# Performance work log

Hardware: AMD Instinct MI355X
Metric: run time of the kernel (lower is better)

Reference implementation:

```python
import jax, jax.numpy as jnp
import numpy as np
from jax import lax

POST_NMS_TOP_N = 1000   # cfg[cfg_key].RPN_POST_NMS_TOP_N
NMS_THRESH = 0.7        # cfg[cfg_key].RPN_NMS_THRESH
NEG = -1e9
B, N = 4, 65536


def setup_inputs() -> dict:
    key = jax.random.key(0)
    k0, k1, k2, k3, k4, k5, k6 = jax.random.split(key, 7)
    scores = jax.random.uniform(k0, (B, N), dtype=jnp.float32)
    # small deltas so exp(dw) stays in a realistic range
    bbox_deltas = 0.1 * jax.random.normal(k1, (B, N, 4), dtype=jnp.float32)
    # plausible anchor boxes inside a 1024x1024 image
    cx = jax.random.uniform(k2, (N,), minval=0.0, maxval=1024.0)
    cy = jax.random.uniform(k3, (N,), minval=0.0, maxval=1024.0)
    w = jax.random.uniform(k4, (N,), minval=16.0, maxval=256.0)
    h = jax.random.uniform(k5, (N,), minval=16.0, maxval=256.0)
    anchors = jnp.stack([cx - 0.5 * w, cy - 0.5 * h, cx + 0.5 * w, cy + 0.5 * h], axis=-1).astype(jnp.float32)
    im_info = jnp.tile(jnp.array([[1024.0, 1024.0, 1.0]], dtype=jnp.float32), (B, 1))
    ids = jax.random.randint(k6, (N,), 0, 5, dtype=jnp.int32)  # FPN level ids
    return {"scores": scores, "bbox_deltas": bbox_deltas, "anchors": anchors,
            "im_info": im_info, "ids": ids}


def _iou_one(box, boxes):
    # box [4], boxes [N,4]; mmcv convention (no +1)
    x1 = jnp.maximum(box[0], boxes[:, 0])
    y1 = jnp.maximum(box[1], boxes[:, 1])
    x2 = jnp.minimum(box[2], boxes[:, 2])
    y2 = jnp.minimum(box[3], boxes[:, 3])
    inter = jnp.clip(x2 - x1, 0.0) * jnp.clip(y2 - y1, 0.0)
    a1 = (box[2] - box[0]) * (box[3] - box[1])
    a2 = (boxes[:, 2] - boxes[:, 0]) * (boxes[:, 3] - boxes[:, 1])
    return inter / jnp.maximum(a1 + a2 - inter, 1e-6)


def _nms_single(boxes, scores, ids):
    # batched_nms: offset boxes by level id so levels never suppress each other
    max_c = jnp.max(boxes) + 1.0
    boxes_off = boxes + (ids.astype(boxes.dtype) * max_c)[:, None]

    def step(s, _):
        i = jnp.argmax(s)
        valid = s[i] > NEG * 0.5
        iou = _iou_one(boxes_off[i], boxes_off)
        s_new = jnp.where(iou > NMS_THRESH, NEG, s).at[i].set(NEG)
        sel = jnp.where(valid, boxes[i], jnp.zeros((4,), boxes.dtype))
        return s_new, sel

    _, sel = lax.scan(step, scores, None, length=POST_NMS_TOP_N)
    return sel  # [POST_NMS_TOP_N, 4], in descending score order (as batched_nms returns)


def _forward(scores, bbox_deltas, anchors, im_info, ids):
    ws = anchors[:, 2] - anchors[:, 0] + 1.0          # [N]
    hs = anchors[:, 3] - anchors[:, 1] + 1.0
    ctr_x = anchors[:, 0] + 0.5 * ws
    ctr_y = anchors[:, 1] + 0.5 * hs
    dx, dy, dw, dh = (bbox_deltas[..., 0], bbox_deltas[..., 1],
                      bbox_deltas[..., 2], bbox_deltas[..., 3])  # [B,N]
    pcx = dx * ws + ctr_x
    pcy = dy * hs + ctr_y
    pw = jnp.exp(dw) * ws
    ph = jnp.exp(dh) * hs
    proposals = jnp.stack([pcx - 0.5 * pw, pcy - 0.5 * ph,
                           pcx + 0.5 * pw, pcy + 0.5 * ph], axis=-1)  # [B,N,4]
    # clip_boxes: x in [0, w-1], y in [0, h-1]
    wmax = im_info[:, 1][:, None] - 1.0
    hmax = im_info[:, 0][:, None] - 1.0
    x1 = jnp.clip(proposals[..., 0], 0.0, wmax)
    y1 = jnp.clip(proposals[..., 1], 0.0, hmax)
    x2 = jnp.clip(proposals[..., 2], 0.0, wmax)
    y2 = jnp.clip(proposals[..., 3], 0.0, hmax)
    proposals = jnp.stack([x1, y1, x2, y2], axis=-1)
    # per-image batched NMS (greedy descending-score selection == sort + NMS)
    sel = jax.vmap(_nms_single, in_axes=(0, 0, None))(proposals, scores, ids)  # [B,topN,4]
    batch_col = jnp.broadcast_to(
        jnp.arange(scores.shape[0], dtype=sel.dtype)[:, None, None],
        (scores.shape[0], POST_NMS_TOP_N, 1))
    return jnp.concatenate([batch_col, sel], axis=-1)  # [B,topN,5]


def reference(scores, bbox_deltas, anchors, im_info, ids):
    return _forward(scores, bbox_deltas, anchors, im_info, ids)
```

## Files before the change

kernel.cpp:

```cpp
#include <hip/hip_runtime.h>
#include <stdint.h>

#define NB     65536
#define BATCH  4
#define TOPN   1000
#define MMAX   2048
#define NTILE  (MMAX / 64)
#define NPAIRS (NTILE * (NTILE + 1) / 2)
#define CAP    128
#define KSUP   8
#define UNC    128
#define THRESH 0.974f
#define NEGV   (-1e9f)
#define NMS_T  0.7f

#define OFF_CBLK   64
#define OFF_KRAW   1088
#define OFF_SBOX   263232
#define OFF_SLEV   394304
#define OFF_CNT2   427072
#define OFF_SUP    459840

__device__ __forceinline__ void decode_box(const float4* __restrict__ anchors4,
                                           const float4* __restrict__ deltas4,
                                           int b, int i, float wmax, float hmax,
                                           float& x1, float& y1, float& x2, float& y2) {
  float4 a = anchors4[i];
  float4 d = deltas4[(size_t)b * NB + i];
  float ws = a.z - a.x + 1.0f;
  float hs = a.w - a.y + 1.0f;
  float cx = a.x + 0.5f * ws;
  float cy = a.y + 0.5f * hs;
  float pcx = d.x * ws + cx;
  float pcy = d.y * hs + cy;
  float pw = expf(d.z) * ws;
  float ph = expf(d.w) * hs;
  x1 = pcx - 0.5f * pw; y1 = pcy - 0.5f * ph;
  x2 = pcx + 0.5f * pw; y2 = pcy + 0.5f * ph;
  x1 = fminf(fmaxf(x1, 0.0f), wmax);
  y1 = fminf(fmaxf(y1, 0.0f), hmax);
  x2 = fminf(fmaxf(x2, 0.0f), wmax);
  y2 = fminf(fmaxf(y2, 0.0f), hmax);
}

__device__ __forceinline__ uint32_t blockscan(uint32_t v, volatile uint32_t* wsum,
                                              int tid, uint32_t* total) {
  __syncthreads();
  int lane = tid & 63, wid = tid >> 6;
  uint32_t x = v;
  for (int off = 1; off < 64; off <<= 1) {
    uint32_t u = __shfl_up(x, off, 64);
    if (lane >= off) x += u;
  }
  if (lane == 63) wsum[wid] = x;
  __syncthreads();
  if (tid == 0) {
    uint32_t run = 0;
    for (int w = 0; w < 4; ++w) { uint32_t t = wsum[w]; wsum[w] = run; run += t; }
    wsum[4] = run;
  }
  __syncthreads();
  *total = wsum[4];
  return x - v + wsum[wid];
}

__global__ __launch_bounds__(256) void k_prep(const float* __restrict__ scores,
                                              unsigned long long* __restrict__ keys_raw,
                                              uint32_t* __restrict__ cnt_blk) {
  const int b = blockIdx.x >> 6;
  const int blk = blockIdx.x & 63;
  const int tid = threadIdx.x;
  __shared__ uint32_t wsum[5];
  const float4* s4 = (const float4*)scores + (size_t)b * (NB / 4) + (size_t)blk * 256 + tid;
  float4 s = *s4;
  float sc4[4] = {s.x, s.y, s.z, s.w};
  uint32_t cmask = 0, ccount = 0;
#pragma unroll
  for (int k = 0; k < 4; ++k)
    if (sc4[k] >= THRESH) { cmask |= (1u << k); ccount++; }
  uint32_t total;
  uint32_t p = blockscan(ccount, wsum, tid, &total);
  if (tid == 0) cnt_blk[blockIdx.x] = total;
  unsigned long long* dst = keys_raw + (size_t)blockIdx.x * CAP;
#pragma unroll
  for (int k = 0; k < 4; ++k) {
    if (cmask & (1u << k)) {
      if (p < (uint32_t)CAP) {
        int i = (blk << 10) + (tid << 2) + k;
        dst[p] = ((unsigned long long)(~__float_as_uint(sc4[k])) << 32) | (uint32_t)i;
      }
      p++;
    }
  }
}

__global__ __launch_bounds__(256) void k_rank(const uint32_t* __restrict__ cnt_blk,
                                              const unsigned long long* __restrict__ keys_raw,
                                              const float4* __restrict__ deltas4,
                                              const float4* __restrict__ anchors4,
                                              const float* __restrict__ im_info,
                                              const int* __restrict__ ids,
                                              uint32_t* ctrs,
                                              float4* sboxes, int* slev,
                                              uint32_t* cnt2) {
  const int b = blockIdx.y;
  const int r = blockIdx.x;
  const int tid = threadIdx.x;
  const int lane = tid & 63, wid = tid >> 6;
  __shared__ unsigned long long sk[MMAX];
  __shared__ uint32_t scnt[64], sbs[64];
  __shared__ uint32_t psum[256];
  __shared__ uint32_t meta[2];

  if (tid < 64) {
    uint32_t c = cnt_blk[b * 64 + tid];
    uint32_t cc = min(c, (uint32_t)CAP);
    scnt[tid] = cc;
    uint32_t x = cc;
    for (int off = 1; off < 64; off <<= 1) {
      uint32_t u = __shfl_up(x, off, 64);
      if (lane >= off) x += u;
    }
    sbs[tid] = x - cc;
    unsigned long long ov = __ballot(c > (uint32_t)CAP);
    if (tid == 63) { meta[0] = x; meta[1] = (ov != 0ULL) ? 1u : 0u; }
  }
  __syncthreads();
  uint32_t nsum = meta[0];
  int n = min((int)nsum, MMAX);
  uint32_t flag = meta[1] | ((nsum > (uint32_t)MMAX) ? 1u : 0u);
  if (r == 0 && tid == 0) {
    ctrs[b] = (uint32_t)n;
    ctrs[8 + b] = flag;
  }
  if (tid < 64) cnt2[(size_t)b * MMAX + r * 64 + tid] = 0u;
  {
    int k = tid >> 2, q = tid & 3;
    uint32_t cb = sbs[k], cc = scnt[k];
    const unsigned long long* src = keys_raw + ((size_t)b * 64 + k) * CAP;
    for (uint32_t o = q; o < cc; o += 4) {
      uint32_t d = cb + o;
      if (d < (uint32_t)MMAX) sk[d] = src[o];
    }
  }
  for (int i = tid; i < MMAX; i += 256) if (i >= n) sk[i] = ~0ULL;
  __syncthreads();
  int c = r * 64 + lane;
  uint32_t partial = 0;
  if (c < n) {
    unsigned long long myk = sk[c];
    const ulonglong2* p2 = (const ulonglong2*)(sk + (size_t)wid * 512);
    for (int it = 0; it < 256; it += 4) {
      ulonglong2 a = p2[it], bq = p2[it + 1], cq = p2[it + 2], dq = p2[it + 3];
      partial += (uint32_t)(a.x < myk) + (uint32_t)(a.y < myk) +
                 (uint32_t)(bq.x < myk) + (uint32_t)(bq.y < myk) +
                 (uint32_t)(cq.x < myk) + (uint32_t)(cq.y < myk) +
                 (uint32_t)(dq.x < myk) + (uint32_t)(dq.y < myk);
    }
  }
  psum[wid * 64 + lane] = partial;
  __syncthreads();
  if (tid < 64) {
    int cc = r * 64 + tid;
    if (cc < n) {
      uint32_t rank = psum[tid] + psum[64 + tid] + psum[128 + tid] + psum[192 + tid];
      if (rank < (uint32_t)MMAX) {
        unsigned long long key = sk[cc];
        int i = (int)(uint32_t)key;
        float wmax = im_info[b * 3 + 1] - 1.0f;
        float hmax = im_info[b * 3 + 0] - 1.0f;
        float x1, y1, x2, y2;
        decode_box(anchors4, deltas4, b, i, wmax, hmax, x1, y1, x2, y2);
        sboxes[(size_t)b * MMAX + rank] = make_float4(x1, y1, x2, y2);
        slev[(size_t)b * MMAX + rank] = ids[i];
      }
    }
  }
}

__global__ __launch_bounds__(64) void k_pairs(uint32_t* ctrs,
                                              const float4* __restrict__ sboxes,
                                              const int* __restrict__ slev,
                                              uint32_t* cnt2, int* suplist) {
  int b = blockIdx.y;
  int p = blockIdx.x;
  int tj = (int)((sqrtf(8.0f * (float)p + 1.0f) - 1.0f) * 0.5f);
  while ((tj + 1) * (tj + 2) / 2 <= p) ++tj;
  while (tj * (tj + 1) / 2 > p) --tj;
  int ti = p - tj * (tj + 1) / 2;
  int n = min((int)ctrs[b], MMAX);
  if (tj * 64 >= n) return;
  int lane = threadIdx.x;

  __shared__ float4 ib[64];
  __shared__ int il[64];
  int ii = ti * 64 + lane;
  if (ii < n) {
    ib[lane] = sboxes[(size_t)b * MMAX + ii];
    il[lane] = slev[(size_t)b * MMAX + ii];
  } else {
    il[lane] = -1;
  }
  int j = tj * 64 + lane;
  float4 J = make_float4(0.f, 0.f, 0.f, 0.f);
  int jl = -2;
  float aj = 0.0f;
  if (j < n) {
    J = sboxes[(size_t)b * MMAX + j];
    jl = slev[(size_t)b * MMAX + j];
    aj = (J.z - J.x) * (J.w - J.y);
  }
  __syncthreads();
  if (j < n) {
    int imax = (ti == tj) ? lane : 64;
    for (int k = 0; k < imax; ++k) {
      if (il[k] != jl) continue;
      float4 I = ib[k];
      float xx1 = fmaxf(I.x, J.x), yy1 = fmaxf(I.y, J.y);
      float xx2 = fminf(I.z, J.z), yy2 = fminf(I.w, J.w);
      float inter = fmaxf(xx2 - xx1, 0.0f) * fmaxf(yy2 - yy1, 0.0f);
      float ai = (I.z - I.x) * (I.w - I.y);
      float iou = inter / fmaxf((ai + aj) - inter, 1e-6f);
      if (iou > NMS_T) {
        uint32_t s = atomicAdd(&cnt2[(size_t)b * MMAX + j], 1u);
        if (s < (uint32_t)KSUP) suplist[((size_t)b * MMAX + j) * KSUP + s] = ti * 64 + k;
        else ctrs[8 + b] = 1u;
      }
    }
  }
}

__device__ __forceinline__ uint32_t scan_pair(uint32_t pairsum, volatile uint32_t* wsum,
                                              int tid, uint32_t* total_out) {
  int lane = tid & 63, wid = tid >> 6;
  uint32_t v = pairsum;
  for (int off = 1; off < 64; off <<= 1) {
    uint32_t u = __shfl_up(v, off, 64);
    if (lane >= off) v += u;
  }
  if (lane == 63) wsum[wid] = v;
  __syncthreads();
  if (tid == 0) {
    uint32_t run = 0;
    for (int w = 0; w < 16; ++w) { uint32_t t = wsum[w]; wsum[w] = run; run += t; }
    wsum[16] = run;
  }
  __syncthreads();
  uint32_t incl = v + wsum[wid];
  *total_out = wsum[16];
  return incl - pairsum;
}

__global__ __launch_bounds__(1024) void k_out(const float* __restrict__ scores,
                                              const float4* __restrict__ deltas4,
                                              const float4* __restrict__ anchors4,
                                              const float* __restrict__ im_info,
                                              const int* __restrict__ ids,
                                              const uint32_t* __restrict__ ctrs,
                                              const uint32_t* __restrict__ cnt2,
                                              const int* __restrict__ suplist,
                                              const float4* __restrict__ sboxes,
                                              float* __restrict__ out) {
  int b = blockIdx.x;
  int tid = threadIdx.x;
  __shared__ uint8_t kept[MMAX];
  __shared__ uint32_t wsum[17];
  __shared__ uint16_t unc[UNC];
  __shared__ int supld[UNC][KSUP];
  __shared__ uint8_t supn[UNC];
  int n = min((int)ctrs[b], MMAX);
  int j0 = tid * 2, j1 = tid * 2 + 1;
  uint32_t c0 = (j0 < n) ? cnt2[(size_t)b * MMAX + j0] : 0u;
  uint32_t c1 = (j1 < n) ? cnt2[(size_t)b * MMAX + j1] : 0u;
  kept[j0] = (j0 < n && c0 == 0u) ? 1 : 0;
  kept[j1] = (j1 < n && c1 == 0u) ? 1 : 0;
  uint32_t u0 = (j0 < n && c0 > 0u) ? 1u : 0u;
  uint32_t u1 = (j1 < n && c1 > 0u) ? 1u : 0u;
  uint32_t tot_unc;
  uint32_t base = scan_pair(u0 + u1, wsum, tid, &tot_unc);
  if (u0) {
    uint32_t p = base;
    if (p < UNC) {
      int m = (int)min(c0, (uint32_t)KSUP);
      unc[p] = (uint16_t)j0; supn[p] = (uint8_t)m;
      for (int s = 0; s < m; ++s) supld[p][s] = suplist[((size_t)b * MMAX + j0) * KSUP + s];
    }
  }
  if (u1) {
    uint32_t p = base + u0;
    if (p < UNC) {
      int m = (int)min(c1, (uint32_t)KSUP);
      unc[p] = (uint16_t)j1; supn[p] = (uint8_t)m;
      for (int s = 0; s < m; ++s) supld[p][s] = suplist[((size_t)b * MMAX + j1) * KSUP + s];
    }
  }
  __syncthreads();
  if (tid < 64) {
    int nu = (int)min(tot_unc, (uint32_t)UNC);
    for (int u = 0; u < nu; ++u) {
      int m = (int)supn[u];
      int pred = (tid < m) ? (int)kept[supld[u][tid]] : 0;
      unsigned long long bal = __ballot(pred);
      if (tid == 0) kept[unc[u]] = (bal == 0ULL) ? 1 : 0;
    }
  }
  __syncthreads();
  uint32_t k0 = kept[j0], k1 = kept[j1];
  uint32_t total;
  uint32_t pbase = scan_pair(k0 + k1, wsum, tid, &total);
  if (k0 && pbase < (uint32_t)TOPN) {
    float4 bx = sboxes[(size_t)b * MMAX + j0];
    size_t o = ((size_t)b * TOPN + pbase) * 5;
    out[o] = (float)b; out[o+1] = bx.x; out[o+2] = bx.y; out[o+3] = bx.z; out[o+4] = bx.w;
  }
  if (k1) {
    uint32_t p = pbase + k0;
    if (p < (uint32_t)TOPN) {
      float4 bx = sboxes[(size_t)b * MMAX + j1];
      size_t o = ((size_t)b * TOPN + p) * 5;
      out[o] = (float)b; out[o+1] = bx.x; out[o+2] = bx.y; out[o+3] = bx.z; out[o+4] = bx.w;
    }
  }
  for (int t = tid; t < TOPN; t += 1024) {
    if ((uint32_t)t >= total) {
      size_t o = ((size_t)b * TOPN + t) * 5;
      out[o] = (float)b; out[o+1] = 0.0f; out[o+2] = 0.0f; out[o+3] = 0.0f; out[o+4] = 0.0f;
    }
  }

  bool needFB = (ctrs[8 + b] != 0u) || (total < (uint32_t)TOPN) || (tot_unc > (uint32_t)UNC);
  if (!needFB) return;

  __shared__ uint32_t mask[NB / 32];
  __shared__ float rv[1024];
  __shared__ int ri[1024];
  __shared__ float fm[16];
  const float wmax = im_info[b * 3 + 1] - 1.0f;
  const float hmax = im_info[b * 3 + 0] - 1.0f;
  __syncthreads();
  float mx = 0.0f;
  for (int i = tid; i < NB; i += 1024) {
    float x1, y1, x2, y2;
    decode_box(anchors4, deltas4, b, i, wmax, hmax, x1, y1, x2, y2);
    mx = fmaxf(mx, fmaxf(fmaxf(x1, y1), fmaxf(x2, y2)));
  }
  for (int o = 32; o > 0; o >>= 1) mx = fmaxf(mx, __shfl_xor(mx, o, 64));
  if ((tid & 63) == 0) fm[tid >> 6] = mx;
  __syncthreads();
  if (tid == 0) {
    float m = fm[0];
    for (int w = 1; w < 16; ++w) m = fmaxf(m, fm[w]);
    fm[0] = m;
  }
  for (int i = tid; i < NB / 32; i += 1024) mask[i] = 0u;
  __syncthreads();
  float max_c = fm[0] + 1.0f;
  for (int it = 0; it < TOPN; ++it) {
    float bv = -3e38f; int bi = 0x7fffffff;
    for (int i = tid; i < NB; i += 1024) {
      bool sup = (mask[i >> 5] >> (i & 31)) & 1u;
      float v = sup ? NEGV : scores[(size_t)b * NB + i];
      if (v > bv || (v == bv && i < bi)) { bv = v; bi = i; }
    }
    rv[tid] = bv; ri[tid] = bi;
    __syncthreads();
    for (int s = 512; s > 0; s >>= 1) {
      if (tid < s) {
        float v2 = rv[tid + s]; int i2 = ri[tid + s];
        if (v2 > rv[tid] || (v2 == rv[tid] && i2 < ri[tid])) { rv[tid] = v2; ri[tid] = i2; }
      }
      __syncthreads();
    }
    int ii = ri[0]; float vv = rv[0];
    bool valid = vv > NEGV * 0.5f;
    if (!valid) {
      if (tid == 0) {
        size_t o = ((size_t)b * TOPN + it) * 5;
        out[o] = (float)b; out[o+1] = 0; out[o+2] = 0; out[o+3] = 0; out[o+4] = 0;
      }
      __syncthreads();
      continue;
    }
    float x1, y1, x2, y2;
    decode_box(anchors4, deltas4, b, ii, wmax, hmax, x1, y1, x2, y2);
    int lv = ids[ii];
    float off = (float)lv * max_c;
    float s0 = x1 + off, s1 = y1 + off, s2 = x2 + off, s3 = y2 + off;
    float a1 = (s2 - s0) * (s3 - s1);
    if (tid == 0) {
      size_t o = ((size_t)b * TOPN + it) * 5;
      out[o] = (float)b; out[o+1] = x1; out[o+2] = y1; out[o+3] = x2; out[o+4] = y2;
    }
    for (int j = tid; j < NB; j += 1024) {
      if ((mask[j >> 5] >> (j & 31)) & 1u) continue;
      if (ids[j] != lv) continue;
      float bx1, by1, bx2, by2;
      decode_box(anchors4, deltas4, b, j, wmax, hmax, bx1, by1, bx2, by2);
      float t0 = bx1 + off, t1 = by1 + off, t2 = bx2 + off, t3 = by2 + off;
      float xx1 = fmaxf(s0, t0), yy1 = fmaxf(s1, t1);
      float xx2 = fminf(s2, t2), yy2 = fminf(s3, t3);
      float inter = fmaxf(xx2 - xx1, 0.0f) * fmaxf(yy2 - yy1, 0.0f);
      float a2r = (t2 - t0) * (t3 - t1);
      float iou = inter / fmaxf(a1 + a2r - inter, 1e-6f);
      if (iou > NMS_T) atomicOr(&mask[j >> 5], 1u << (j & 31));
    }
    if (tid == 0) atomicOr(&mask[ii >> 5], 1u << (ii & 31));
    __syncthreads();
  }
}

extern "C" void kernel_launch(void* const* d_in, const int* in_sizes, int n_in,
                              void* d_out, int out_size, void* d_ws, size_t ws_size,
                              hipStream_t stream) {
  const float*  scores   = (const float*)d_in[0];
  const float4* deltas4  = (const float4*)d_in[1];
  const float4* anchors4 = (const float4*)d_in[2];
  const float*  im_info  = (const float*)d_in[3];
  const int*    ids      = (const int*)d_in[4];
  float* out = (float*)d_out;

  char* ws = (char*)d_ws;
  uint32_t*           ctrs     = (uint32_t*)ws;
  uint32_t*           cnt_blk  = (uint32_t*)(ws + OFF_CBLK);
  unsigned long long* keys_raw = (unsigned long long*)(ws + OFF_KRAW);
  float4*             sboxes   = (float4*)(ws + OFF_SBOX);
  int*                slev     = (int*)(ws + OFF_SLEV);
  uint32_t*           cnt2     = (uint32_t*)(ws + OFF_CNT2);
  int*                suplist  = (int*)(ws + OFF_SUP);

  hipLaunchKernelGGL(k_prep, dim3(64 * BATCH), dim3(256), 0, stream,
                     scores, keys_raw, cnt_blk);
  hipLaunchKernelGGL(k_rank, dim3(NTILE, BATCH), dim3(256), 0, stream,
                     cnt_blk, keys_raw, deltas4, anchors4, im_info, ids,
                     ctrs, sboxes, slev, cnt2);
  hipLaunchKernelGGL(k_pairs, dim3(NPAIRS, BATCH), dim3(64), 0, stream,
                     ctrs, sboxes, slev, cnt2, suplist);
  hipLaunchKernelGGL(k_out, dim3(BATCH), dim3(1024), 0, stream,
                     scores, deltas4, anchors4, im_info, ids, ctrs, cnt2, suplist,
                     sboxes, out);
}
```

Measured before the change: 100.7 us.

## Fuse four NMS kernels into one persistent kernel with grid barriers

Replaces the four separate launches (prep, rank, pairwise IoU, output) with one persistent 256-block kernel that uses software grid-wide barriers between phases, plus a tiny init kernel that resets the barrier counters. The pairwise stage now runs as warp-level tasks and broadcasts boxes with shuffles instead of shared memory, and the output stage uses 256 threads instead of 1024. The aim is to remove inter-kernel launch gaps and tail effects. In exchange it relies on all 256 blocks being co-resident, which a large shared-memory footprint could break, and it slows the fallback path, which now runs with fewer threads.

```diff
diff --git a/kernel.cpp b/kernel.cpp
--- a/kernel.cpp
+++ b/kernel.cpp
@@ -13,6 +13,7 @@
 #define THRESH 0.974f
 #define NEGV   (-1e9f)
 #define NMS_T  0.7f
+#define GRIDN  256
 
 #define OFF_CBLK   64
 #define OFF_KRAW   1088
@@ -64,348 +65,354 @@
   return x - v + wsum[wid];
 }
 
-__global__ __launch_bounds__(256) void k_prep(const float* __restrict__ scores,
-                                              unsigned long long* __restrict__ keys_raw,
-                                              uint32_t* __restrict__ cnt_blk) {
-  const int b = blockIdx.x >> 6;
-  const int blk = blockIdx.x & 63;
-  const int tid = threadIdx.x;
-  __shared__ uint32_t wsum[5];
-  const float4* s4 = (const float4*)scores + (size_t)b * (NB / 4) + (size_t)blk * 256 + tid;
-  float4 s = *s4;
-  float sc4[4] = {s.x, s.y, s.z, s.w};
-  uint32_t cmask = 0, ccount = 0;
-#pragma unroll
-  for (int k = 0; k < 4; ++k)
-    if (sc4[k] >= THRESH) { cmask |= (1u << k); ccount++; }
-  uint32_t total;
-  uint32_t p = blockscan(ccount, wsum, tid, &total);
-  if (tid == 0) cnt_blk[blockIdx.x] = total;
-  unsigned long long* dst = keys_raw + (size_t)blockIdx.x * CAP;
-#pragma unroll
-  for (int k = 0; k < 4; ++k) {
-    if (cmask & (1u << k)) {
-      if (p < (uint32_t)CAP) {
-        int i = (blk << 10) + (tid << 2) + k;
-        dst[p] = ((unsigned long long)(~__float_as_uint(sc4[k])) << 32) | (uint32_t)i;
-      }
-      p++;
-    }
-  }
-}
-
-__global__ __launch_bounds__(256) void k_rank(const uint32_t* __restrict__ cnt_blk,
-                                              const unsigned long long* __restrict__ keys_raw,
-                                              const float4* __restrict__ deltas4,
-                                              const float4* __restrict__ anchors4,
-                                              const float* __restrict__ im_info,
-                                              const int* __restrict__ ids,
-                                              uint32_t* ctrs,
-                                              float4* sboxes, int* slev,
-                                              uint32_t* cnt2) {
-  const int b = blockIdx.y;
-  const int r = blockIdx.x;
+__device__ __forceinline__ void gbar(uint32_t* cnt, uint32_t* gen, int tid) {
+  __syncthreads();
+  if (tid == 0) {
+    __threadfence();
+    uint32_t g = __hip_atomic_load(gen, __ATOMIC_RELAXED, __HIP_MEMORY_SCOPE_AGENT);
+    uint32_t a = __hip_atomic_fetch_add(cnt, 1u, __ATOMIC_ACQ_REL, __HIP_MEMORY_SCOPE_AGENT);
+    if (a == (uint32_t)(GRIDN - 1)) {
+      __hip_atomic_store(cnt, 0u, __ATOMIC_RELAXED, __HIP_MEMORY_SCOPE_AGENT);
+      __hip_atomic_fetch_add(gen, 1u, __ATOMIC_RELEASE, __HIP_MEMORY_SCOPE_AGENT);
+    } else {
+      while (__hip_atomic_load(gen, __ATOMIC_ACQUIRE, __HIP_MEMORY_SCOPE_AGENT) == g)
+        __builtin_amdgcn_s_sleep(2);
+    }
+    __threadfence();
+  }
+  __syncthreads();
+}
+
+__global__ void k_init(uint32_t* ctrs) {
+  if (threadIdx.x < 2)
+    __hip_atomic_store(&ctrs[12 + threadIdx.x], 0u, __ATOMIC_RELAXED,
+                       __HIP_MEMORY_SCOPE_AGENT);
+}
+
+__global__ __launch_bounds__(256) void k_fused(
+    const float* __restrict__ scores, const float4* __restrict__ deltas4,
+    const float4* __restrict__ anchors4, const float* __restrict__ im_info,
+    const int* __restrict__ ids,
+    unsigned long long* __restrict__ keys_raw, uint32_t* __restrict__ cnt_blk,
+    uint32_t* ctrs, float4* __restrict__ sboxes, int* __restrict__ slev,
+    uint32_t* __restrict__ cnt2, int* __restrict__ suplist,
+    float* __restrict__ out) {
+  const int bid = blockIdx.x;
   const int tid = threadIdx.x;
   const int lane = tid & 63, wid = tid >> 6;
+  uint32_t* bar_cnt = &ctrs[12];
+  uint32_t* bar_gen = &ctrs[13];
+
+  __shared__ uint32_t wsum[17];
   __shared__ unsigned long long sk[MMAX];
   __shared__ uint32_t scnt[64], sbs[64];
   __shared__ uint32_t psum[256];
   __shared__ uint32_t meta[2];
-
-  if (tid < 64) {
-    uint32_t c = cnt_blk[b * 64 + tid];
-    uint32_t cc = min(c, (uint32_t)CAP);
-    scnt[tid] = cc;
-    uint32_t x = cc;
-    for (int off = 1; off < 64; off <<= 1) {
-      uint32_t u = __shfl_up(x, off, 64);
-      if (lane >= off) x += u;
-    }
-    sbs[tid] = x - cc;
-    unsigned long long ov = __ballot(c > (uint32_t)CAP);
-    if (tid == 63) { meta[0] = x; meta[1] = (ov != 0ULL) ? 1u : 0u; }
-  }
-  __syncthreads();
-  uint32_t nsum = meta[0];
-  int n = min((int)nsum, MMAX);
-  uint32_t flag = meta[1] | ((nsum > (uint32_t)MMAX) ? 1u : 0u);
-  if (r == 0 && tid == 0) {
-    ctrs[b] = (uint32_t)n;
-    ctrs[8 + b] = flag;
-  }
-  if (tid < 64) cnt2[(size_t)b * MMAX + r * 64 + tid] = 0u;
+  __shared__ uint8_t  kept[MMAX];
+  __shared__ uint16_t unc[UNC];
+  __shared__ int      supld[UNC][KSUP];
+  __shared__ uint8_t  supn[UNC];
+  __shared__ uint32_t mask[NB / 32];
+  __shared__ float    rv[256];
+  __shared__ int      ri[256];
+  __shared__ float    fm[4];
+
   {
-    int k = tid >> 2, q = tid & 3;
-    uint32_t cb = sbs[k], cc = scnt[k];
-    const unsigned long long* src = keys_raw + ((size_t)b * 64 + k) * CAP;
-    for (uint32_t o = q; o < cc; o += 4) {
-      uint32_t d = cb + o;
-      if (d < (uint32_t)MMAX) sk[d] = src[o];
-    }
-  }
-  for (int i = tid; i < MMAX; i += 256) if (i >= n) sk[i] = ~0ULL;
-  __syncthreads();
-  int c = r * 64 + lane;
-  uint32_t partial = 0;
-  if (c < n) {
-    unsigned long long myk = sk[c];
-    const ulonglong2* p2 = (const ulonglong2*)(sk + (size_t)wid * 512);
-    for (int it = 0; it < 256; it += 4) {
-      ulonglong2 a = p2[it], bq = p2[it + 1], cq = p2[it + 2], dq = p2[it + 3];
-      partial += (uint32_t)(a.x < myk) + (uint32_t)(a.y < myk) +
-                 (uint32_t)(bq.x < myk) + (uint32_t)(bq.y < myk) +
-                 (uint32_t)(cq.x < myk) + (uint32_t)(cq.y < myk) +
-                 (uint32_t)(dq.x < myk) + (uint32_t)(dq.y < myk);
-    }
-  }
-  psum[wid * 64 + lane] = partial;
-  __syncthreads();
-  if (tid < 64) {
-    int cc = r * 64 + tid;
-    if (cc < n) {
-      uint32_t rank = psum[tid] + psum[64 + tid] + psum[128 + tid] + psum[192 + tid];
-      if (rank < (uint32_t)MMAX) {
-        unsigned long long key = sk[cc];
-        int i = (int)(uint32_t)key;
-        float wmax = im_info[b * 3 + 1] - 1.0f;
-        float hmax = im_info[b * 3 + 0] - 1.0f;
+    const int b = bid >> 6;
+    const int blk = bid & 63;
+    const float4* s4 = (const float4*)scores + (size_t)b * (NB / 4) + (size_t)blk * 256 + tid;
+    float4 s = *s4;
+    float sc4[4] = {s.x, s.y, s.z, s.w};
+    uint32_t cmask = 0, ccount = 0;
+#pragma unroll
+    for (int k = 0; k < 4; ++k)
+      if (sc4[k] >= THRESH) { cmask |= (1u << k); ccount++; }
+    uint32_t total;
+    uint32_t p = blockscan(ccount, wsum, tid, &total);
+    if (tid == 0) cnt_blk[bid] = total;
+    unsigned long long* dst = keys_raw + (size_t)bid * CAP;
+#pragma unroll
+    for (int k = 0; k < 4; ++k) {
+      if (cmask & (1u << k)) {
+        if (p < (uint32_t)CAP) {
+          int i = (blk << 10) + (tid << 2) + k;
+          dst[p] = ((unsigned long long)(~__float_as_uint(sc4[k])) << 32) | (uint32_t)i;
+        }
+        p++;
+      }
+    }
+  }
+
+  gbar(bar_cnt, bar_gen, tid);
+
+  if (bid < NTILE * BATCH) {
+    const int b = bid >> 5;
+    const int r = bid & 31;
+    if (tid < 64) {
+      uint32_t c = cnt_blk[b * 64 + tid];
+      uint32_t cc = min(c, (uint32_t)CAP);
+      scnt[tid] = cc;
+      uint32_t x = cc;
+      for (int off = 1; off < 64; off <<= 1) {
+        uint32_t u = __shfl_up(x, off, 64);
+        if (lane >= off) x += u;
+      }
+      sbs[tid] = x - cc;
+      unsigned long long ov = __ballot(c > (uint32_t)CAP);
+      if (tid == 63) { meta[0] = x; meta[1] = (ov != 0ULL) ? 1u : 0u; }
+    }
+    __syncthreads();
+    uint32_t nsum = meta[0];
+    int n = min((int)nsum, MMAX);
+    uint32_t flag = meta[1] | ((nsum > (uint32_t)MMAX) ? 1u : 0u);
+    if (r == 0 && tid == 0) {
+      ctrs[b] = (uint32_t)n;
+      ctrs[8 + b] = flag;
+    }
+    if (tid < 64) cnt2[(size_t)b * MMAX + r * 64 + tid] = 0u;
+    {
+      int k = tid >> 2, q = tid & 3;
+      uint32_t cb = sbs[k], cc = scnt[k];
+      const unsigned long long* src = keys_raw + ((size_t)b * 64 + k) * CAP;
+      for (uint32_t o = q; o < cc; o += 4) {
+        uint32_t d = cb + o;
+        if (d < (uint32_t)MMAX) sk[d] = src[o];
+      }
+    }
+    for (int i = tid; i < MMAX; i += 256) if (i >= n) sk[i] = ~0ULL;
+    __syncthreads();
+    int c = r * 64 + lane;
+    uint32_t partial = 0;
+    if (c < n) {
+      unsigned long long myk = sk[c];
+      const ulonglong2* p2 = (const ulonglong2*)(sk + (size_t)wid * 512);
+      for (int it = 0; it < 256; it += 4) {
+        ulonglong2 a = p2[it], bq = p2[it + 1], cq = p2[it + 2], dq = p2[it + 3];
+        partial += (uint32_t)(a.x < myk) + (uint32_t)(a.y < myk) +
+                   (uint32_t)(bq.x < myk) + (uint32_t)(bq.y < myk) +
+                   (uint32_t)(cq.x < myk) + (uint32_t)(cq.y < myk) +
+                   (uint32_t)(dq.x < myk) + (uint32_t)(dq.y < myk);
+      }
+    }
+    psum[wid * 64 + lane] = partial;
+    __syncthreads();
+    if (tid < 64) {
+      int cc = r * 64 + tid;
+      if (cc < n) {
+        uint32_t rank = psum[tid] + psum[64 + tid] + psum[128 + tid] + psum[192 + tid];
+        if (rank < (uint32_t)MMAX) {
+          unsigned long long key = sk[cc];
+          int i = (int)(uint32_t)key;
+          float wmax = im_info[b * 3 + 1] - 1.0f;
+          float hmax = im_info[b * 3 + 0] - 1.0f;
+          float x1, y1, x2, y2;
+          decode_box(anchors4, deltas4, b, i, wmax, hmax, x1, y1, x2, y2);
+          sboxes[(size_t)b * MMAX + rank] = make_float4(x1, y1, x2, y2);
+          slev[(size_t)b * MMAX + rank] = ids[i];
+        }
+      }
+    }
+  }
+
+  gbar(bar_cnt, bar_gen, tid);
+
+  {
+    const int gwid = bid * 4 + wid;
+    for (int t = gwid; t < NPAIRS * BATCH; t += 1024) {
+      const int b = t & 3;
+      const int p = t >> 2;
+      int tj = (int)((sqrtf(8.0f * (float)p + 1.0f) - 1.0f) * 0.5f);
+      while ((tj + 1) * (tj + 2) / 2 <= p) ++tj;
+      while (tj * (tj + 1) / 2 > p) --tj;
+      int ti = p - tj * (tj + 1) / 2;
+      int n = min((int)ctrs[b], MMAX);
+      if (tj * 64 >= n) continue;
+
+      int ii = ti * 64 + lane;
+      float4 I = make_float4(0.f, 0.f, 0.f, 0.f);
+      int ilv = -1;
+      if (ii < n) {
+        I = sboxes[(size_t)b * MMAX + ii];
+        ilv = slev[(size_t)b * MMAX + ii];
+      }
+      int j = tj * 64 + lane;
+      bool jv = (j < n);
+      float4 J = make_float4(0.f, 0.f, 0.f, 0.f);
+      int jl = -2;
+      float aj = 0.0f;
+      if (jv) {
+        J = sboxes[(size_t)b * MMAX + j];
+        jl = slev[(size_t)b * MMAX + j];
+        aj = (J.z - J.x) * (J.w - J.y);
+      }
+      int imax = (ti == tj) ? lane : 64;
+      for (int k = 0; k < 64; ++k) {
+        int   kl = __shfl(ilv, k, 64);
+        float Ix = __shfl(I.x, k, 64);
+        float Iy = __shfl(I.y, k, 64);
+        float Iz = __shfl(I.z, k, 64);
+        float Iw = __shfl(I.w, k, 64);
+        if (!jv || k >= imax || kl != jl) continue;
+        float xx1 = fmaxf(Ix, J.x), yy1 = fmaxf(Iy, J.y);
+        float xx2 = fminf(Iz, J.z), yy2 = fminf(Iw, J.w);
+        float inter = fmaxf(xx2 - xx1, 0.0f) * fmaxf(yy2 - yy1, 0.0f);
+        float ai = (Iz - Ix) * (Iw - Iy);
+        float iou = inter / fmaxf((ai + aj) - inter, 1e-6f);
+        if (iou > NMS_T) {
+          uint32_t s = atomicAdd(&cnt2[(size_t)b * MMAX + j], 1u);
+          if (s < (uint32_t)KSUP) suplist[((size_t)b * MMAX + j) * KSUP + s] = ti * 64 + k;
+          else atomicOr(&ctrs[8 + b], 1u);
+        }
+      }
+    }
+  }
+
+  gbar(bar_cnt, bar_gen, tid);
+
+  if (bid < BATCH) {
+    const int b = bid;
+    int n = min((int)ctrs[b], MMAX);
+    const int jb = tid * 8;
+    uint32_t cj[8];
+    uint32_t uf = 0, usum = 0;
+#pragma unroll
+    for (int k = 0; k < 8; ++k) {
+      int j = jb + k;
+      uint32_t c = (j < n) ? cnt2[(size_t)b * MMAX + j] : 0u;
+      cj[k] = c;
+      kept[j] = (j < n && c == 0u) ? 1 : 0;
+      uint32_t u = (j < n && c > 0u) ? 1u : 0u;
+      uf |= (u << k); usum += u;
+    }
+    uint32_t tot_unc;
+    uint32_t base = blockscan(usum, wsum, tid, &tot_unc);
+    {
+      uint32_t p = base;
+#pragma unroll
+      for (int k = 0; k < 8; ++k) {
+        if ((uf >> k) & 1u) {
+          if (p < (uint32_t)UNC) {
+            int j = jb + k;
+            int m = (int)min(cj[k], (uint32_t)KSUP);
+            unc[p] = (uint16_t)j; supn[p] = (uint8_t)m;
+            for (int s = 0; s < m; ++s)
+              supld[p][s] = suplist[((size_t)b * MMAX + j) * KSUP + s];
+          }
+          p++;
+        }
+      }
+    }
+    __syncthreads();
+    if (tid < 64) {
+      int nu = (int)min(tot_unc, (uint32_t)UNC);
+      for (int u = 0; u < nu; ++u) {
+        int m = (int)supn[u];
+        int pred = (tid < m) ? (int)kept[supld[u][tid]] : 0;
+        unsigned long long bal = __ballot(pred);
+        if (tid == 0) kept[unc[u]] = (bal == 0ULL) ? 1 : 0;
+      }
+    }
+    __syncthreads();
+    uint32_t kf = 0, ksum = 0;
+#pragma unroll
+    for (int k = 0; k < 8; ++k) {
+      uint32_t kk = kept[jb + k];
+      kf |= (kk << k); ksum += kk;
+    }
+    uint32_t total;
+    uint32_t pb = blockscan(ksum, wsum, tid, &total);
+    {
+      uint32_t p = pb;
+#pragma unroll
+      for (int k = 0; k < 8; ++k) {
+        if ((kf >> k) & 1u) {
+          if (p < (uint32_t)TOPN) {
+            float4 bx = sboxes[(size_t)b * MMAX + jb + k];
+            size_t o = ((size_t)b * TOPN + p) * 5;
+            out[o] = (float)b; out[o+1] = bx.x; out[o+2] = bx.y; out[o+3] = bx.z; out[o+4] = bx.w;
+          }
+          p++;
+        }
+      }
+    }
+    for (int t = tid; t < TOPN; t += 256) {
+      if ((uint32_t)t >= total) {
+        size_t o = ((size_t)b * TOPN + t) * 5;
+        out[o] = (float)b; out[o+1] = 0.0f; out[o+2] = 0.0f; out[o+3] = 0.0f; out[o+4] = 0.0f;
+      }
+    }
+
+    bool needFB = (ctrs[8 + b] != 0u) || (total < (uint32_t)TOPN) || (tot_unc > (uint32_t)UNC);
+    if (needFB) {
+      const float wmax = im_info[b * 3 + 1] - 1.0f;
+      const float hmax = im_info[b * 3 + 0] - 1.0f;
+      __syncthreads();
+      float mx = 0.0f;
+      for (int i = tid; i < NB; i += 256) {
         float x1, y1, x2, y2;
         decode_box(anchors4, deltas4, b, i, wmax, hmax, x1, y1, x2, y2);
-        sboxes[(size_t)b * MMAX + rank] = make_float4(x1, y1, x2, y2);
-        slev[(size_t)b * MMAX + rank] = ids[i];
-      }
-    }
-  }
-}
-
-__global__ __launch_bounds__(64) void k_pairs(uint32_t* ctrs,
-                                              const float4* __restrict__ sboxes,
-                                              const int* __restrict__ slev,
-                                              uint32_t* cnt2, int* suplist) {
-  int b = blockIdx.y;
-  int p = blockIdx.x;
-  int tj = (int)((sqrtf(8.0f * (float)p + 1.0f) - 1.0f) * 0.5f);
-  while ((tj + 1) * (tj + 2) / 2 <= p) ++tj;
-  while (tj * (tj + 1) / 2 > p) --tj;
-  int ti = p - tj * (tj + 1) / 2;
-  int n = min((int)ctrs[b], MMAX);
-  if (tj * 64 >= n) return;
-  int lane = threadIdx.x;
-
-  __shared__ float4 ib[64];
-  __shared__ int il[64];
-  int ii = ti * 64 + lane;
-  if (ii < n) {
-    ib[lane] = sboxes[(size_t)b * MMAX + ii];
-    il[lane] = slev[(size_t)b * MMAX + ii];
-  } else {
-    il[lane] = -1;
-  }
-  int j = tj * 64 + lane;
-  float4 J = make_float4(0.f, 0.f, 0.f, 0.f);
-  int jl = -2;
-  float aj = 0.0f;
-  if (j < n) {
-    J = sboxes[(size_t)b * MMAX + j];
-    jl = slev[(size_t)b * MMAX + j];
-    aj = (J.z - J.x) * (J.w - J.y);
-  }
-  __syncthreads();
-  if (j < n) {
-    int imax = (ti == tj) ? lane : 64;
-    for (int k = 0; k < imax; ++k) {
-      if (il[k] != jl) continue;
-      float4 I = ib[k];
-      float xx1 = fmaxf(I.x, J.x), yy1 = fmaxf(I.y, J.y);
-      float xx2 = fminf(I.z, J.z), yy2 = fminf(I.w, J.w);
-      float inter = fmaxf(xx2 - xx1, 0.0f) * fmaxf(yy2 - yy1, 0.0f);
-      float ai = (I.z - I.x) * (I.w - I.y);
-      float iou = inter / fmaxf((ai + aj) - inter, 1e-6f);
-      if (iou > NMS_T) {
-        uint32_t s = atomicAdd(&cnt2[(size_t)b * MMAX + j], 1u);
-        if (s < (uint32_t)KSUP) suplist[((size_t)b * MMAX + j) * KSUP + s] = ti * 64 + k;
-        else ctrs[8 + b] = 1u;
-      }
-    }
-  }
-}
-
-__device__ __forceinline__ uint32_t scan_pair(uint32_t pairsum, volatile uint32_t* wsum,
-                                              int tid, uint32_t* total_out) {
-  int lane = tid & 63, wid = tid >> 6;
-  uint32_t v = pairsum;
-  for (int off = 1; off < 64; off <<= 1) {
-    uint32_t u = __shfl_up(v, off, 64);
-    if (lane >= off) v += u;
-  }
-  if (lane == 63) wsum[wid] = v;
-  __syncthreads();
-  if (tid == 0) {
-    uint32_t run = 0;
-    for (int w = 0; w < 16; ++w) { uint32_t t = wsum[w]; wsum[w] = run; run += t; }
-    wsum[16] = run;
-  }
-  __syncthreads();
-  uint32_t incl = v + wsum[wid];
-  *total_out = wsum[16];
-  return incl - pairsum;
-}
-
-__global__ __launch_bounds__(1024) void k_out(const float* __restrict__ scores,
-                                              const float4* __restrict__ deltas4,
-                                              const float4* __restrict__ anchors4,
-                                              const float* __restrict__ im_info,
-                                              const int* __restrict__ ids,
-                                              const uint32_t* __restrict__ ctrs,
-                                              const uint32_t* __restrict__ cnt2,
-                                              const int* __restrict__ suplist,
-                                              const float4* __restrict__ sboxes,
-                                              float* __restrict__ out) {
-  int b = blockIdx.x;
-  int tid = threadIdx.x;
-  __shared__ uint8_t kept[MMAX];
-  __shared__ uint32_t wsum[17];
-  __shared__ uint16_t unc[UNC];
-  __shared__ int supld[UNC][KSUP];
-  __shared__ uint8_t supn[UNC];
-  int n = min((int)ctrs[b], MMAX);
-  int j0 = tid * 2, j1 = tid * 2 + 1;
-  uint32_t c0 = (j0 < n) ? cnt2[(size_t)b * MMAX + j0] : 0u;
-  uint32_t c1 = (j1 < n) ? cnt2[(size_t)b * MMAX + j1] : 0u;
-  kept[j0] = (j0 < n && c0 == 0u) ? 1 : 0;
-  kept[j1] = (j1 < n && c1 == 0u) ? 1 : 0;
-  uint32_t u0 = (j0 < n && c0 > 0u) ? 1u : 0u;
-  uint32_t u1 = (j1 < n && c1 > 0u) ? 1u : 0u;
-  uint32_t tot_unc;
-  uint32_t base = scan_pair(u0 + u1, wsum, tid, &tot_unc);
-  if (u0) {
-    uint32_t p = base;
-    if (p < UNC) {
-      int m = (int)min(c0, (uint32_t)KSUP);
-      unc[p] = (uint16_t)j0; supn[p] = (uint8_t)m;
-      for (int s = 0; s < m; ++s) supld[p][s] = suplist[((size_t)b * MMAX + j0) * KSUP + s];
-    }
-  }
-  if (u1) {
-    uint32_t p = base + u0;
-    if (p < UNC) {
-      int m = (int)min(c1, (uint32_t)KSUP);
-      unc[p] = (uint16_t)j1; supn[p] = (uint8_t)m;
-      for (int s = 0; s < m; ++s) supld[p][s] = suplist[((size_t)b * MMAX + j1) * KSUP + s];
-    }
-  }
-  __syncthreads();
-  if (tid < 64) {
-    int nu = (int)min(tot_unc, (uint32_t)UNC);
-    for (int u = 0; u < nu; ++u) {
-      int m = (int)supn[u];
-      int pred = (tid < m) ? (int)kept[supld[u][tid]] : 0;
-      unsigned long long bal = __ballot(pred);
-      if (tid == 0) kept[unc[u]] = (bal == 0ULL) ? 1 : 0;
-    }
-  }
-  __syncthreads();
-  uint32_t k0 = kept[j0], k1 = kept[j1];
-  uint32_t total;
-  uint32_t pbase = scan_pair(k0 + k1, wsum, tid, &total);
-  if (k0 && pbase < (uint32_t)TOPN) {
-    float4 bx = sboxes[(size_t)b * MMAX + j0];
-    size_t o = ((size_t)b * TOPN + pbase) * 5;
-    out[o] = (float)b; out[o+1] = bx.x; out[o+2] = bx.y; out[o+3] = bx.z; out[o+4] = bx.w;
-  }
-  if (k1) {
-    uint32_t p = pbase + k0;
-    if (p < (uint32_t)TOPN) {
-      float4 bx = sboxes[(size_t)b * MMAX + j1];
-      size_t o = ((size_t)b * TOPN + p) * 5;
-      out[o] = (float)b; out[o+1] = bx.x; out[o+2] = bx.y; out[o+3] = bx.z; out[o+4] = bx.w;
-    }
-  }
-  for (int t = tid; t < TOPN; t += 1024) {
-    if ((uint32_t)t >= total) {
-      size_t o = ((size_t)b * TOPN + t) * 5;
-      out[o] = (float)b; out[o+1] = 0.0f; out[o+2] = 0.0f; out[o+3] = 0.0f; out[o+4] = 0.0f;
-    }
-  }
-
-  bool needFB = (ctrs[8 + b] != 0u) || (total < (uint32_t)TOPN) || (tot_unc > (uint32_t)UNC);
-  if (!needFB) return;
-
-  __shared__ uint32_t mask[NB / 32];
-  __shared__ float rv[1024];
-  __shared__ int ri[1024];
-  __shared__ float fm[16];
-  const float wmax = im_info[b * 3 + 1] - 1.0f;
-  const float hmax = im_info[b * 3 + 0] - 1.0f;
-  __syncthreads();
-  float mx = 0.0f;
-  for (int i = tid; i < NB; i += 1024) {
-    float x1, y1, x2, y2;
-    decode_box(anchors4, deltas4, b, i, wmax, hmax, x1, y1, x2, y2);
-    mx = fmaxf(mx, fmaxf(fmaxf(x1, y1), fmaxf(x2, y2)));
-  }
-  for (int o = 32; o > 0; o >>= 1) mx = fmaxf(mx, __shfl_xor(mx, o, 64));
-  if ((tid & 63) == 0) fm[tid >> 6] = mx;
-  __syncthreads();
-  if (tid == 0) {
-    float m = fm[0];
-    for (int w = 1; w < 16; ++w) m = fmaxf(m, fm[w]);
-    fm[0] = m;
-  }
-  for (int i = tid; i < NB / 32; i += 1024) mask[i] = 0u;
-  __syncthreads();
-  float max_c = fm[0] + 1.0f;
-  for (int it = 0; it < TOPN; ++it) {
-    float bv = -3e38f; int bi = 0x7fffffff;
-    for (int i = tid; i < NB; i += 1024) {
-      bool sup = (mask[i >> 5] >> (i & 31)) & 1u;
-      float v = sup ? NEGV : scores[(size_t)b * NB + i];
-      if (v > bv || (v == bv && i < bi)) { bv = v; bi = i; }
-    }
-    rv[tid] = bv; ri[tid] = bi;
-    __syncthreads();
-    for (int s = 512; s > 0; s >>= 1) {
-      if (tid < s) {
-        float v2 = rv[tid + s]; int i2 = ri[tid + s];
-        if (v2 > rv[tid] || (v2 == rv[tid] && i2 < ri[tid])) { rv[tid] = v2; ri[tid] = i2; }
-      }
+        mx = fmaxf(mx, fmaxf(fmaxf(x1, y1), fmaxf(x2, y2)));
+      }
+      for (int o = 32; o > 0; o >>= 1) mx = fmaxf(mx, __shfl_xor(mx, o, 64));
+      if ((tid & 63) == 0) fm[tid >> 6] = mx;
       __syncthreads();
-    }
-    int ii = ri[0]; float vv = rv[0];
-    bool valid = vv > NEGV * 0.5f;
-    if (!valid) {
-      if (tid == 0) {
-        size_t o = ((size_t)b * TOPN + it) * 5;
-        out[o] = (float)b; out[o+1] = 0; out[o+2] = 0; out[o+3] = 0; out[o+4] = 0;
-      }
+      if (tid == 0) fm[0] = fmaxf(fmaxf(fm[0], fm[1]), fmaxf(fm[2], fm[3]));
+      for (int i = tid; i < NB / 32; i += 256) mask[i] = 0u;
       __syncthreads();
-      continue;
-    }
-    float x1, y1, x2, y2;
-    decode_box(anchors4, deltas4, b, ii, wmax, hmax, x1, y1, x2, y2);
-    int lv = ids[ii];
-    float off = (float)lv * max_c;
-    float s0 = x1 + off, s1 = y1 + off, s2 = x2 + off, s3 = y2 + off;
-    float a1 = (s2 - s0) * (s3 - s1);
-    if (tid == 0) {
-      size_t o = ((size_t)b * TOPN + it) * 5;
-      out[o] = (float)b; out[o+1] = x1; out[o+2] = y1; out[o+3] = x2; out[o+4] = y2;
-    }
-    for (int j = tid; j < NB; j += 1024) {
-      if ((mask[j >> 5] >> (j & 31)) & 1u) continue;
-      if (ids[j] != lv) continue;
-      float bx1, by1, bx2, by2;
-      decode_box(anchors4, deltas4, b, j, wmax, hmax, bx1, by1, bx2, by2);
-      float t0 = bx1 + off, t1 = by1 + off, t2 = bx2 + off, t3 = by2 + off;
-      float xx1 = fmaxf(s0, t0), yy1 = fmaxf(s1, t1);
-      float xx2 = fminf(s2, t2), yy2 = fminf(s3, t3);
-      float inter = fmaxf(xx2 - xx1, 0.0f) * fmaxf(yy2 - yy1, 0.0f);
-      float a2r = (t2 - t0) * (t3 - t1);
-      float iou = inter / fmaxf(a1 + a2r - inter, 1e-6f);
-      if (iou > NMS_T) atomicOr(&mask[j >> 5], 1u << (j & 31));
-    }
-    if (tid == 0) atomicOr(&mask[ii >> 5], 1u << (ii & 31));
-    __syncthreads();
+      float max_c = fm[0] + 1.0f;
+      for (int it = 0; it < TOPN; ++it) {
+        float bv = -3e38f; int bi = 0x7fffffff;
+        for (int i = tid; i < NB; i += 256) {
+          bool sup = (mask[i >> 5] >> (i & 31)) & 1u;
+          float v = sup ? NEGV : scores[(size_t)b * NB + i];
+          if (v > bv || (v == bv && i < bi)) { bv = v; bi = i; }
+        }
+        rv[tid] = bv; ri[tid] = bi;
+        __syncthreads();
+        for (int s = 128; s > 0; s >>= 1) {
+          if (tid < s) {
+            float v2 = rv[tid + s]; int i2 = ri[tid + s];
+            if (v2 > rv[tid] || (v2 == rv[tid] && i2 < ri[tid])) { rv[tid] = v2; ri[tid] = i2; }
+          }
+          __syncthreads();
+        }
+        int ii = ri[0]; float vv = rv[0];
+        bool valid = vv > NEGV * 0.5f;
+        if (!valid) {
+          if (tid == 0) {
+            size_t o = ((size_t)b * TOPN + it) * 5;
+            out[o] = (float)b; out[o+1] = 0; out[o+2] = 0; out[o+3] = 0; out[o+4] = 0;
+          }
+          __syncthreads();
+          continue;
+        }
+        float x1, y1, x2, y2;
+        decode_box(anchors4, deltas4, b, ii, wmax, hmax, x1, y1, x2, y2);
+        int lv = ids[ii];
+        float off = (float)lv * max_c;
+        float s0 = x1 + off, s1 = y1 + off, s2 = x2 + off, s3 = y2 + off;
+        float a1 = (s2 - s0) * (s3 - s1);
+        if (tid == 0) {
+          size_t o = ((size_t)b * TOPN + it) * 5;
+          out[o] = (float)b; out[o+1] = x1; out[o+2] = y1; out[o+3] = x2; out[o+4] = y2;
+        }
+        for (int j = tid; j < NB; j += 256) {
+          if ((mask[j >> 5] >> (j & 31)) & 1u) continue;
+          if (ids[j] != lv) continue;
+          float bx1, by1, bx2, by2;
+          decode_box(anchors4, deltas4, b, j, wmax, hmax, bx1, by1, bx2, by2);
+          float t0 = bx1 + off, t1 = by1 + off, t2 = bx2 + off, t3 = by2 + off;
+          float xx1 = fmaxf(s0, t0), yy1 = fmaxf(s1, t1);
+          float xx2 = fminf(s2, t2), yy2 = fminf(s3, t3);
+          float inter = fmaxf(xx2 - xx1, 0.0f) * fmaxf(yy2 - yy1, 0.0f);
+          float a2r = (t2 - t0) * (t3 - t1);
+          float iou = inter / fmaxf(a1 + a2r - inter, 1e-6f);
+          if (iou > NMS_T) atomicOr(&mask[j >> 5], 1u << (j & 31));
+        }
+        if (tid == 0) atomicOr(&mask[ii >> 5], 1u << (ii & 31));
+        __syncthreads();
+      }
+    }
   }
 }
 
@@ -428,14 +435,8 @@
   uint32_t*           cnt2     = (uint32_t*)(ws + OFF_CNT2);
   int*                suplist  = (int*)(ws + OFF_SUP);
 
-  hipLaunchKernelGGL(k_prep, dim3(64 * BATCH), dim3(256), 0, stream,
-                     scores, keys_raw, cnt_blk);
-  hipLaunchKernelGGL(k_rank, dim3(NTILE, BATCH), dim3(256), 0, stream,
-                     cnt_blk, keys_raw, deltas4, anchors4, im_info, ids,
-                     ctrs, sboxes, slev, cnt2);
-  hipLaunchKernelGGL(k_pairs, dim3(NPAIRS, BATCH), dim3(64), 0, stream,
-                     ctrs, sboxes, slev, cnt2, suplist);
-  hipLaunchKernelGGL(k_out, dim3(BATCH), dim3(1024), 0, stream,
-                     scores, deltas4, anchors4, im_info, ids, ctrs, cnt2, suplist,
-                     sboxes, out);
-}
+  hipLaunchKernelGGL(k_init, dim3(1), dim3(64), 0, stream, ctrs);
+  hipLaunchKernelGGL(k_fused, dim3(GRIDN), dim3(256), 0, stream,
+                     scores, deltas4, anchors4, im_info, ids,
+                     keys_raw, cnt_blk, ctrs, sboxes, slev, cnt2, suplist, out);
+}
```

After: 206.0 us. +104.7%, slower.
